# Performance work log

Measured on AMD Instinct MI355X. Metric: run time of the kernel, lower is better.

The kernel has to match this reference:

```python
import jax, jax.numpy as jnp
import numpy as np

N_FFT = 512
HOP = N_FFT // 4  # torch.stft default hop_length
SR = 16000
SS = 340.4
DIST = 1.0


def _hann(n):
    # torch.hann_window default is periodic
    return (0.5 * (1.0 - jnp.cos(2.0 * jnp.pi * jnp.arange(n) / n))).astype(jnp.float32)


def _stft(x):
    # x: [N, L] -> complex [N, F, T]; matches torch.stft(center=True, pad_mode='reflect', onesided=True)
    pad = N_FFT // 2
    xp = jnp.pad(x, ((0, 0), (pad, pad)), mode='reflect')
    T = (xp.shape[1] - N_FFT) // HOP + 1
    idx = jnp.arange(T)[:, None] * HOP + jnp.arange(N_FFT)[None, :]  # [T, n_fft]
    frames = xp[:, idx] * _hann(N_FFT)[None, None, :]                # [N, T, n_fft]
    X = jnp.fft.rfft(frames, axis=-1)                                # [N, T, F]
    return jnp.swapaxes(X, 1, 2)                                     # [N, F, T]


def setup_inputs() -> dict:
    key = jax.random.key(0)
    k1, k2, k3 = jax.random.split(key, 3)
    B, C, L = 16, 4, 160000
    x = jax.random.normal(k1, (B, C, L), dtype=jnp.float32)
    angle = jax.random.uniform(k2, (B, 1), dtype=jnp.float32) * 360.0
    mic_pos = jax.random.normal(k3, (B, C, 3), dtype=jnp.float32) * 0.05
    return {"x": x, "angle": angle, "mic_pos": mic_pos}


def reference(x, angle, mic_pos):
    B, C, L = x.shape
    X = _stft(x.reshape(B * C, L))            # [B*C, F, T] complex
    Fdim, T = X.shape[1], X.shape[2]
    X = X.reshape(B, C, Fdim, T)

    # 'X' feature: real/imag concat over channel dim -> [B, 2C, F, T]
    featX = jnp.concatenate([X.real, X.imag], axis=1)

    # 'SV' feature: steering vectors
    ang = angle[:, 0]
    half_pi = jnp.float32(np.pi / 2)
    sin90 = jnp.sin(half_pi)
    cos90 = jnp.cos(half_pi)  # ~0, kept for faithfulness
    rad = -ang * (jnp.pi / 180.0)
    loc_src = jnp.stack([
        DIST * jnp.cos(rad) * sin90,
        DIST * jnp.sin(rad) * sin90,
        jnp.full_like(ang, DIST * cos90),
    ], axis=1)  # [B, 3]

    # Original computes torch.norm over the FULL [B,3] difference per mic i (a scalar),
    # so TDOA is identical across batch: Frobenius norm over (B, 3) axes.
    TDOA = jnp.sqrt(jnp.sum((mic_pos - loc_src[:, None, :]) ** 2, axis=(0, 2)))  # [C]
    TDOA = TDOA - TDOA[0]
    TDOA = jnp.broadcast_to(TDOA[None, :], (B, C))  # [B, C]

    # Steering[b,c,f] = exp(f * TDOA[b,c] * const), const = -1j*2*pi*sr/(n_fft*ss)
    coef = -2.0 * jnp.pi * SR / (N_FFT * SS)
    phase = coef * jnp.arange(Fdim, dtype=jnp.float32)[None, None, :] * TDOA[:, :, None]  # [B,C,F]
    sv = jnp.exp(1j * phase)  # complex64, unit magnitude
    sv = sv / jnp.linalg.norm(sv, axis=1, keepdims=True)  # normalize over channels
    sv = jnp.broadcast_to(sv[..., None], (B, C, Fdim, T))
    featSV = jnp.concatenate([sv.real, sv.imag], axis=1)  # [B, 2C, F, T]

    feature = jnp.concatenate([featX, featSV], axis=1)    # [B, 4C, F, T]
    feature = feature.reshape(B, 4 * C * Fdim, T)
    return jnp.transpose(feature, (0, 2, 1))               # [B, T, 4C*F]
```

## Files before the change

### kernel.cpp

```cpp
#include <hip/hip_runtime.h>
#include <math.h>

#define L_SIG 160000
#define HOPC 128
#define FD 257
#define TDIM 1251
#define ROW 4112
#define NROWS (16 * TDIM)
#define NBC 64
#define NFR (NBC * TDIM)
#define NPAIR (NFR / 2)

typedef float floatx4 __attribute__((ext_vector_type(4)));


__global__ __launch_bounds__(256) void setup_kernel(const float* __restrict__ angle,
                                                    const float* __restrict__ mic,
                                                    float* __restrict__ tbl) {
    int tid = threadIdx.x;
    __shared__ float tdoa[4];
    if (tid == 0) {
        const float half_pi = (float)(M_PI / 2.0);
        float s90 = sinf(half_pi);
        float c90 = cosf(half_pi);
        float acc0 = 0.f, acc1 = 0.f, acc2 = 0.f, acc3 = 0.f;
        for (int b = 0; b < 16; ++b) {
            float ang = angle[b];
            float rad = -ang * (float)(M_PI / 180.0);
            float lx = cosf(rad) * s90;
            float ly = sinf(rad) * s90;
            float lz = c90;
            #pragma unroll
            for (int c = 0; c < 4; ++c) {
                const float* m = mic + ((size_t)b * 4 + c) * 3;
                float dx = m[0] - lx, dy = m[1] - ly, dz = m[2] - lz;
                float s = dx * dx + dy * dy + dz * dz;
                if (c == 0) acc0 += s; else if (c == 1) acc1 += s;
                else if (c == 2) acc2 += s; else acc3 += s;
            }
        }
        float t0 = sqrtf(acc0);
        tdoa[0] = 0.0f;
        tdoa[1] = sqrtf(acc1) - t0;
        tdoa[2] = sqrtf(acc2) - t0;
        tdoa[3] = sqrtf(acc3) - t0;
    }
    __syncthreads();
    const float coef = (float)(-2.0 * M_PI * 16000.0 / (512.0 * 340.4));
    for (int i = tid; i < 4 * FD; i += 256) {
        int c = i / FD;
        int f = i - c * FD;
        float ph = coef * (float)f * tdoa[c];
        tbl[i]        = cosf(ph) * 0.5f;
        tbl[1028 + i] = sinf(ph) * 0.5f;
    }
}

__device__ __forceinline__ void bfly8(float (&zr)[8], float (&zi)[8]) {
    const float C = 0.70710678118654752440f;
    float sr0=zr[0]+zr[4], si0=zi[0]+zi[4], dr0=zr[0]-zr[4], di0=zi[0]-zi[4];
    float sr1=zr[1]+zr[5], si1=zi[1]+zi[5], dr1=zr[1]-zr[5], di1=zi[1]-zi[5];
    float sr2=zr[2]+zr[6], si2=zi[2]+zi[6], dr2=zr[2]-zr[6], di2=zi[2]-zi[6];
    float sr3=zr[3]+zr[7], si3=zi[3]+zi[7], dr3=zr[3]-zr[7], di3=zi[3]-zi[7];
    float t;
    t = C*(dr1+di1); di1 = C*(di1-dr1); dr1 = t;
    t = dr2; dr2 = di2; di2 = -t;
    t = C*(di3-dr3); di3 = -C*(dr3+di3); dr3 = t;
    float p0r=sr0+sr2, p0i=si0+si2, p1r=sr1+sr3, p1i=si1+si3;
    float q0r=sr0-sr2, q0i=si0-si2, q1r=sr1-sr3, q1i=si1-si3;
    zr[0]=p0r+p1r; zi[0]=p0i+p1i;
    zr[2]=q0r+q1i; zi[2]=q0i-q1r;
    zr[4]=p0r-p1r; zi[4]=p0i-p1i;
    zr[6]=q0r-q1i; zi[6]=q0i+q1r;
    p0r=dr0+dr2; p0i=di0+di2; p1r=dr1+dr3; p1i=di1+di3;
    q0r=dr0-dr2; q0i=di0-di2; q1r=dr1-dr3; q1i=di1-di3;
    zr[1]=p0r+p1r; zi[1]=p0i+p1i;
    zr[3]=q0r+q1i; zi[3]=q0i-q1r;
    zr[5]=p0r-p1r; zi[5]=p0i-p1i;
    zr[7]=q0r-q1i; zi[7]=q0i+q1r;
}

__device__ __forceinline__ void cmul(float& r, float& i, float ar, float ai, float br, float bi) {
    r = ar * br - ai * bi;
    i = ar * bi + ai * br;
}

__device__ __forceinline__ void twiddle8(float (&zr)[8], float (&zi)[8], float wr, float wi) {
    float p2r, p2i, p3r, p3i, p4r, p4i, p5r, p5i, p6r, p6i, p7r, p7i;
    cmul(p2r, p2i, wr, wi, wr, wi);
    cmul(p3r, p3i, p2r, p2i, wr, wi);
    cmul(p4r, p4i, p2r, p2i, p2r, p2i);
    cmul(p5r, p5i, p4r, p4i, wr, wi);
    cmul(p6r, p6i, p3r, p3i, p3r, p3i);
    cmul(p7r, p7i, p4r, p4i, p3r, p3i);
    float t;
    t = zr[1]*wr - zi[1]*wi;  zi[1] = zr[1]*wi + zi[1]*wr;  zr[1] = t;
    t = zr[2]*p2r - zi[2]*p2i; zi[2] = zr[2]*p2i + zi[2]*p2r; zr[2] = t;
    t = zr[3]*p3r - zi[3]*p3i; zi[3] = zr[3]*p3i + zi[3]*p3r; zr[3] = t;
    t = zr[4]*p4r - zi[4]*p4i; zi[4] = zr[4]*p4i + zi[4]*p4r; zr[4] = t;
    t = zr[5]*p5r - zi[5]*p5i; zi[5] = zr[5]*p5i + zi[5]*p5r; zr[5] = t;
    t = zr[6]*p6r - zi[6]*p6i; zi[6] = zr[6]*p6i + zi[6]*p6r; zr[6] = t;
    t = zr[7]*p7r - zi[7]*p7i; zi[7] = zr[7]*p7i + zi[7]*p7r; zr[7] = t;
}

#define PHYS(i) ((i) + ((i) >> 3))

__global__ __launch_bounds__(256) void stft8_kernel(const float* __restrict__ x,
                                                    const float* __restrict__ tbl,
                                                    float* __restrict__ out) {
    __shared__ float2 exch[4][576];
    const int tid = threadIdx.x;
    const int wv  = tid >> 6;
    const int j   = tid & 63;
    const int pid = blockIdx.x * 4 + wv;
    const int fid0 = 2 * pid;
    const int fid1 = fid0 + 1;
    const int t0 = fid0 % TDIM, bc0 = fid0 / TDIM;
    const int t1 = fid1 % TDIM, bc1 = fid1 / TDIM;

    const float PI_256 = 0.012271846303085129838f;
    float sj, cj;
    __sincosf((float)j * PI_256, &sj, &cj);
    const float R2 = 0.70710678118654752440f;
    float cv[8];
    cv[0] = cj;            cv[1] = (cj - sj) * R2;
    cv[2] = -sj;           cv[3] = (-cj - sj) * R2;
    cv[4] = -cj;           cv[5] = (sj - cj) * R2;
    cv[6] = sj;            cv[7] = (cj + sj) * R2;

    const float* xs0 = x + (size_t)bc0 * L_SIG;
    const float* xs1 = x + (size_t)bc1 * L_SIG;
    const int g0 = t0 * HOPC - 256 + j;
    const int g1 = t1 * HOPC - 256 + j;
    float zr[8], zi[8];

    const bool in0 = (t0 >= 2) && (t0 < 1249);
    const bool in1 = (t1 >= 2) && (t1 < 1249);
    if (in0 && in1) {
        #pragma unroll
        for (int r = 0; r < 8; ++r) {
            float w = 0.5f - 0.5f * cv[r];
            zr[r] = xs0[g0 + 64 * r] * w;
            zi[r] = xs1[g1 + 64 * r] * w;
        }
    } else {
        #pragma unroll
        for (int r = 0; r < 8; ++r) {
            int a0 = g0 + 64 * r; a0 = (a0 < 0) ? -a0 : a0; if (a0 >= L_SIG) a0 = 2 * L_SIG - 2 - a0;
            int a1 = g1 + 64 * r; a1 = (a1 < 0) ? -a1 : a1; if (a1 >= L_SIG) a1 = 2 * L_SIG - 2 - a1;
            float w = 0.5f - 0.5f * cv[r];
            zr[r] = xs0[a0] * w;
            zi[r] = xs1[a1] * w;
        }
    }

    float2* buf = exch[wv];

    bfly8(zr, zi);
    twiddle8(zr, zi, cj, -sj);
    #pragma unroll
    for (int k = 0; k < 8; ++k) {
        int idx = 8 * j + k;
        buf[PHYS(idx)] = make_float2(zr[k], zi[k]);
    }
    #pragma unroll
    for (int r = 0; r < 8; ++r) {
        int idx = j + 64 * r;
        float2 v = buf[PHYS(idx)];
        zr[r] = v.x; zi[r] = v.y;
    }

    bfly8(zr, zi);
    float s1v, c1v;
    __sincosf((float)(j & ~7) * PI_256, &s1v, &c1v);
    twiddle8(zr, zi, c1v, -s1v);
    #pragma unroll
    for (int k = 0; k < 8; ++k) {
        int idx = 64 * (j >> 3) + (j & 7) + 8 * k;
        buf[PHYS(idx)] = make_float2(zr[k], zi[k]);
    }
    #pragma unroll
    for (int r = 0; r < 8; ++r) {
        int idx = j + 64 * r;
        float2 v = buf[PHYS(idx)];
        zr[r] = v.x; zi[r] = v.y;
    }

    bfly8(zr, zi);

    const int srcl = (64 - j) & 63;
    float pr_[8], pi_[8];
    #pragma unroll
    for (int m = 0; m < 8; ++m) {
        pr_[m] = __shfl(zr[m], srcl, 64);
        pi_[m] = __shfl(zi[m], srcl, 64);
    }

    const int b0 = bc0 >> 2, c0 = bc0 & 3;
    const int b1 = bc1 >> 2, c1 = bc1 & 3;
    const size_t base0 = ((size_t)b0 * TDIM + t0) * ROW + (size_t)c0 * FD;
    const size_t base1 = ((size_t)b1 * TDIM + t1) * ROW + (size_t)c1 * FD;
    const bool l0 = (j == 0);

    #pragma unroll
    for (int k = 0; k < 5; ++k) {
        float Pr = l0 ? pr_[(8 - k) & 7] : pr_[7 - k];
        float Pi = l0 ? pi_[(8 - k) & 7] : pi_[7 - k];
        float F0r = 0.5f * (zr[k] + Pr);
        float F0i = 0.5f * (zi[k] - Pi);
        float F1r = 0.5f * (zi[k] + Pi);
        float F1i = 0.5f * (Pr - zr[k]);
        int f = j + 64 * k;
        if (k < 4 || l0) {
            __builtin_nontemporal_store(F0r, out + base0 + f);
            __builtin_nontemporal_store(F0i, out + base0 + 1028 + f);
            __builtin_nontemporal_store(F1r, out + base1 + f);
            __builtin_nontemporal_store(F1i, out + base1 + 1028 + f);
        }
    }

    const floatx4* S4 = (const floatx4*)tbl;
    if (c0 == 0) {
        floatx4* dst = (floatx4*)(out + base0 + 2056);
        #pragma unroll
        for (int it = 0; it < 8; ++it) {
            int i4 = 64 * it + j;
            __builtin_nontemporal_store(S4[i4], dst + i4);
        }
        if (j < 2)
            __builtin_nontemporal_store(S4[512 + j], dst + 512 + j);
    }
    if (c1 == 0) {
        floatx4* dst = (floatx4*)(out + base1 + 2056);
        #pragma unroll
        for (int it = 0; it < 8; ++it) {
            int i4 = 64 * it + j;
            __builtin_nontemporal_store(S4[i4], dst + i4);
        }
        if (j < 2)
            __builtin_nontemporal_store(S4[512 + j], dst + 512 + j);
    }
}

extern "C" void kernel_launch(void* const* d_in, const int* in_sizes, int n_in,
                              void* d_out, int out_size, void* d_ws, size_t ws_size,
                              hipStream_t stream) {
    const float* x     = (const float*)d_in[0];
    const float* angle = (const float*)d_in[1];
    const float* mic   = (const float*)d_in[2];
    float* out = (float*)d_out;
    float* tbl = (float*)d_ws;

    setup_kernel<<<1, 256, 0, stream>>>(angle, mic, tbl);
    stft8_kernel<<<NPAIR / 4, 256, 0, stream>>>(x, tbl, out);
}
```

Measured before the change: 430.0 us.

## Compute one output row per wavefront and stage it for coalesced vector stores

Each wavefront now handles one (batch, time) row and computes all four channel FFTs as two real-pair 512-point FFTs. The spectra go into LDS so the full 4112-float output row is written with contiguous float4 nontemporal stores, together with the steering table. Before, each wavefront wrote scattered scalar stores into two different rows. In exchange, reflect-index math now runs on every frame, each wavefront holds more registers and does more serial work, and there are half as many wavefronts in total.

```diff
diff --git a/kernel.cpp b/kernel.cpp
--- a/kernel.cpp
+++ b/kernel.cpp
@@ -7,9 +7,6 @@
 #define TDIM 1251
 #define ROW 4112
 #define NROWS (16 * TDIM)
-#define NBC 64
-#define NFR (NBC * TDIM)
-#define NPAIR (NFR / 2)
 
 typedef float floatx4 __attribute__((ext_vector_type(4)));
 
@@ -105,141 +102,138 @@
 
 #define PHYS(i) ((i) + ((i) >> 3))
 
-__global__ __launch_bounds__(256) void stft8_kernel(const float* __restrict__ x,
-                                                    const float* __restrict__ tbl,
-                                                    float* __restrict__ out) {
-    __shared__ float2 exch[4][576];
+__device__ __forceinline__ void fft512_pair(const float* __restrict__ xs0,
+                                            const float* __restrict__ xs1,
+                                            const int (&a)[8], const float (&w8)[8],
+                                            float cj, float sj, float c1v, float s1v,
+                                            int j, float2* buf,
+                                            float (&F0r)[5], float (&F0i)[5],
+                                            float (&F1r)[5], float (&F1i)[5]) {
+    float zr[8], zi[8];
+    #pragma unroll
+    for (int r = 0; r < 8; ++r) {
+        zr[r] = xs0[a[r]] * w8[r];
+        zi[r] = xs1[a[r]] * w8[r];
+    }
+
+    bfly8(zr, zi);
+    twiddle8(zr, zi, cj, -sj);
+    #pragma unroll
+    for (int k = 0; k < 8; ++k) buf[PHYS(8 * j + k)] = make_float2(zr[k], zi[k]);
+    #pragma unroll
+    for (int r = 0; r < 8; ++r) {
+        float2 v = buf[PHYS(j + 64 * r)];
+        zr[r] = v.x; zi[r] = v.y;
+    }
+
+    bfly8(zr, zi);
+    twiddle8(zr, zi, c1v, -s1v);
+    #pragma unroll
+    for (int k = 0; k < 8; ++k) buf[PHYS(64 * (j >> 3) + (j & 7) + 8 * k)] = make_float2(zr[k], zi[k]);
+    #pragma unroll
+    for (int r = 0; r < 8; ++r) {
+        float2 v = buf[PHYS(j + 64 * r)];
+        zr[r] = v.x; zi[r] = v.y;
+    }
+
+    bfly8(zr, zi);
+
+    const int srcl = (64 - j) & 63;
+    float pr_[8], pi_[8];
+    #pragma unroll
+    for (int m = 0; m < 8; ++m) {
+        pr_[m] = __shfl(zr[m], srcl, 64);
+        pi_[m] = __shfl(zi[m], srcl, 64);
+    }
+    const bool l0 = (j == 0);
+    #pragma unroll
+    for (int k = 0; k < 5; ++k) {
+        float Pr = l0 ? pr_[(8 - k) & 7] : pr_[7 - k];
+        float Pi = l0 ? pi_[(8 - k) & 7] : pi_[7 - k];
+        F0r[k] = 0.5f * (zr[k] + Pr);
+        F0i[k] = 0.5f * (zi[k] - Pi);
+        F1r[k] = 0.5f * (zi[k] + Pi);
+        F1i[k] = 0.5f * (Pr - zr[k]);
+    }
+}
+
+__global__ __launch_bounds__(256) void stft_row_kernel(const float* __restrict__ x,
+                                                       const float* __restrict__ tbl,
+                                                       float* __restrict__ out) {
+    __shared__ floatx4 stg4[4][516];
     const int tid = threadIdx.x;
     const int wv  = tid >> 6;
     const int j   = tid & 63;
-    const int pid = blockIdx.x * 4 + wv;
-    const int fid0 = 2 * pid;
-    const int fid1 = fid0 + 1;
-    const int t0 = fid0 % TDIM, bc0 = fid0 / TDIM;
-    const int t1 = fid1 % TDIM, bc1 = fid1 / TDIM;
+    const int wid = blockIdx.x * 4 + wv;
+    const int b = wid / TDIM;
+    const int t = wid - b * TDIM;
 
     const float PI_256 = 0.012271846303085129838f;
     float sj, cj;
     __sincosf((float)j * PI_256, &sj, &cj);
     const float R2 = 0.70710678118654752440f;
-    float cv[8];
-    cv[0] = cj;            cv[1] = (cj - sj) * R2;
-    cv[2] = -sj;           cv[3] = (-cj - sj) * R2;
-    cv[4] = -cj;           cv[5] = (sj - cj) * R2;
-    cv[6] = sj;            cv[7] = (cj + sj) * R2;
-
-    const float* xs0 = x + (size_t)bc0 * L_SIG;
-    const float* xs1 = x + (size_t)bc1 * L_SIG;
-    const int g0 = t0 * HOPC - 256 + j;
-    const int g1 = t1 * HOPC - 256 + j;
-    float zr[8], zi[8];
-
-    const bool in0 = (t0 >= 2) && (t0 < 1249);
-    const bool in1 = (t1 >= 2) && (t1 < 1249);
-    if (in0 && in1) {
-        #pragma unroll
-        for (int r = 0; r < 8; ++r) {
-            float w = 0.5f - 0.5f * cv[r];
-            zr[r] = xs0[g0 + 64 * r] * w;
-            zi[r] = xs1[g1 + 64 * r] * w;
-        }
-    } else {
-        #pragma unroll
-        for (int r = 0; r < 8; ++r) {
-            int a0 = g0 + 64 * r; a0 = (a0 < 0) ? -a0 : a0; if (a0 >= L_SIG) a0 = 2 * L_SIG - 2 - a0;
-            int a1 = g1 + 64 * r; a1 = (a1 < 0) ? -a1 : a1; if (a1 >= L_SIG) a1 = 2 * L_SIG - 2 - a1;
-            float w = 0.5f - 0.5f * cv[r];
-            zr[r] = xs0[a0] * w;
-            zi[r] = xs1[a1] * w;
-        }
-    }
-
-    float2* buf = exch[wv];
-
-    bfly8(zr, zi);
-    twiddle8(zr, zi, cj, -sj);
-    #pragma unroll
-    for (int k = 0; k < 8; ++k) {
-        int idx = 8 * j + k;
-        buf[PHYS(idx)] = make_float2(zr[k], zi[k]);
-    }
-    #pragma unroll
-    for (int r = 0; r < 8; ++r) {
-        int idx = j + 64 * r;
-        float2 v = buf[PHYS(idx)];
-        zr[r] = v.x; zi[r] = v.y;
-    }
-
-    bfly8(zr, zi);
+    float w8[8];
+    w8[0] = 0.5f - 0.5f * cj;
+    w8[1] = 0.5f - 0.5f * ((cj - sj) * R2);
+    w8[2] = 0.5f + 0.5f * sj;
+    w8[3] = 0.5f - 0.5f * ((-cj - sj) * R2);
+    w8[4] = 0.5f + 0.5f * cj;
+    w8[5] = 0.5f - 0.5f * ((sj - cj) * R2);
+    w8[6] = 0.5f - 0.5f * sj;
+    w8[7] = 0.5f - 0.5f * ((cj + sj) * R2);
     float s1v, c1v;
     __sincosf((float)(j & ~7) * PI_256, &s1v, &c1v);
-    twiddle8(zr, zi, c1v, -s1v);
-    #pragma unroll
-    for (int k = 0; k < 8; ++k) {
-        int idx = 64 * (j >> 3) + (j & 7) + 8 * k;
-        buf[PHYS(idx)] = make_float2(zr[k], zi[k]);
-    }
-    #pragma unroll
-    for (int r = 0; r < 8; ++r) {
-        int idx = j + 64 * r;
-        float2 v = buf[PHYS(idx)];
-        zr[r] = v.x; zi[r] = v.y;
-    }
-
-    bfly8(zr, zi);
-
-    const int srcl = (64 - j) & 63;
-    float pr_[8], pi_[8];
-    #pragma unroll
-    for (int m = 0; m < 8; ++m) {
-        pr_[m] = __shfl(zr[m], srcl, 64);
-        pi_[m] = __shfl(zi[m], srcl, 64);
-    }
-
-    const int b0 = bc0 >> 2, c0 = bc0 & 3;
-    const int b1 = bc1 >> 2, c1 = bc1 & 3;
-    const size_t base0 = ((size_t)b0 * TDIM + t0) * ROW + (size_t)c0 * FD;
-    const size_t base1 = ((size_t)b1 * TDIM + t1) * ROW + (size_t)c1 * FD;
-    const bool l0 = (j == 0);
+
+    const int g = t * HOPC - 256 + j;
+    int a[8];
+    #pragma unroll
+    for (int r = 0; r < 8; ++r) {
+        int ar = g + 64 * r;
+        ar = (ar < 0) ? -ar : ar;
+        if (ar >= L_SIG) ar = 2 * L_SIG - 2 - ar;
+        a[r] = ar;
+    }
+
+    float* stg  = (float*)&stg4[wv][0];
+    float2* buf = (float2*)stg;
+
+    const float* xb = x + (size_t)b * 4 * L_SIG;
+    float A0r[5], A0i[5], A1r[5], A1i[5];
+    float B0r[5], B0i[5], B1r[5], B1i[5];
+    fft512_pair(xb,             xb + L_SIG,     a, w8, cj, sj, c1v, s1v, j, buf, A0r, A0i, A1r, A1i);
+    fft512_pair(xb + 2 * L_SIG, xb + 3 * L_SIG, a, w8, cj, sj, c1v, s1v, j, buf, B0r, B0i, B1r, B1i);
 
     #pragma unroll
     for (int k = 0; k < 5; ++k) {
-        float Pr = l0 ? pr_[(8 - k) & 7] : pr_[7 - k];
-        float Pi = l0 ? pi_[(8 - k) & 7] : pi_[7 - k];
-        float F0r = 0.5f * (zr[k] + Pr);
-        float F0i = 0.5f * (zi[k] - Pi);
-        float F1r = 0.5f * (zi[k] + Pi);
-        float F1i = 0.5f * (Pr - zr[k]);
         int f = j + 64 * k;
-        if (k < 4 || l0) {
-            __builtin_nontemporal_store(F0r, out + base0 + f);
-            __builtin_nontemporal_store(F0i, out + base0 + 1028 + f);
-            __builtin_nontemporal_store(F1r, out + base1 + f);
-            __builtin_nontemporal_store(F1i, out + base1 + 1028 + f);
+        if (k < 4 || j == 0) {
+            stg[f]        = A0r[k];
+            stg[257 + f]  = A1r[k];
+            stg[514 + f]  = B0r[k];
+            stg[771 + f]  = B1r[k];
+            stg[1028 + f] = A0i[k];
+            stg[1285 + f] = A1i[k];
+            stg[1542 + f] = B0i[k];
+            stg[1799 + f] = B1i[k];
         }
     }
 
-    const floatx4* S4 = (const floatx4*)tbl;
-    if (c0 == 0) {
-        floatx4* dst = (floatx4*)(out + base0 + 2056);
-        #pragma unroll
-        for (int it = 0; it < 8; ++it) {
-            int i4 = 64 * it + j;
-            __builtin_nontemporal_store(S4[i4], dst + i4);
-        }
-        if (j < 2)
-            __builtin_nontemporal_store(S4[512 + j], dst + 512 + j);
-    }
-    if (c1 == 0) {
-        floatx4* dst = (floatx4*)(out + base1 + 2056);
-        #pragma unroll
-        for (int it = 0; it < 8; ++it) {
-            int i4 = 64 * it + j;
-            __builtin_nontemporal_store(S4[i4], dst + i4);
-        }
-        if (j < 2)
-            __builtin_nontemporal_store(S4[512 + j], dst + 512 + j);
-    }
+    const floatx4* sp = (const floatx4*)stg;
+    floatx4* dst = (floatx4*)(out + (size_t)wid * ROW);
+    #pragma unroll
+    for (int it = 0; it < 8; ++it) {
+        int i4 = 64 * it + j;
+        __builtin_nontemporal_store(sp[i4], dst + i4);
+    }
+    if (j < 2) __builtin_nontemporal_store(sp[512 + j], dst + 512 + j);
+
+    const floatx4* T4 = (const floatx4*)tbl;
+    #pragma unroll
+    for (int it = 0; it < 8; ++it) {
+        int i4 = 64 * it + j;
+        __builtin_nontemporal_store(T4[i4], dst + 514 + i4);
+    }
+    if (j < 2) __builtin_nontemporal_store(T4[512 + j], dst + 514 + 512 + j);
 }
 
 extern "C" void kernel_launch(void* const* d_in, const int* in_sizes, int n_in,
@@ -252,5 +246,5 @@
     float* tbl = (float*)d_ws;
 
     setup_kernel<<<1, 256, 0, stream>>>(angle, mic, tbl);
-    stft8_kernel<<<NPAIR / 4, 256, 0, stream>>>(x, tbl, out);
-}
+    stft_row_kernel<<<NROWS / 4, 256, 0, stream>>>(x, tbl, out);
+}
```

Measured after the change: 367.7 us. 1.17x faster.
